# Kernel optimization log

Measured on AMD Instinct MI355X. Metric: run time of the kernel, lower is better.

Reference implementation:

```python
import jax, jax.numpy as jnp
import numpy as np

N_NODES = 50000
N_EDGES = 1600000
IN_DIM = 128
N_HEADS = 8
OUT_DIM = 16  # output_dim // n_heads = 128 // 8


def setup_inputs() -> dict:
    key = jax.random.key(0)
    ks = jax.random.split(key, 8)
    feature = jax.random.normal(ks[0], (N_NODES, IN_DIM), dtype=jnp.float32)
    edge_src = jax.random.randint(ks[1], (N_EDGES,), 0, N_NODES)
    edge_dst = jax.random.randint(ks[2], (N_EDGES,), 0, N_NODES)
    edge_weight = jax.random.uniform(ks[3], (N_EDGES,), dtype=jnp.float32)
    w_lin = jax.random.normal(ks[4], (IN_DIM, N_HEADS * OUT_DIM), dtype=jnp.float32) * 0.1
    att_l = jax.random.normal(ks[5], (N_HEADS, OUT_DIM), dtype=jnp.float32) * 0.1
    att_r = jax.random.normal(ks[6], (N_HEADS, OUT_DIM), dtype=jnp.float32) * 0.1
    w_res = jax.random.normal(ks[7], (IN_DIM, N_HEADS * OUT_DIM), dtype=jnp.float32) * 0.1
    return {"feature": feature, "edge_src": edge_src, "edge_dst": edge_dst,
            "edge_weight": edge_weight, "w_lin": w_lin, "att_l": att_l,
            "att_r": att_r, "w_res": w_res}


def reference(feature, edge_src, edge_dst, edge_weight, w_lin, att_l, att_r, w_res):
    N = feature.shape[0]
    H, C = att_l.shape
    # Linear projection -> [N, H, C]
    x = (feature @ w_lin).reshape(N, H, C)
    # Per-node attention logits [N, H]
    al = jnp.einsum('nhc,hc->nh', x, att_l)
    ar = jnp.einsum('nhc,hc->nh', x, att_r)
    # Per-edge logits: gather src/dst, weight, leaky-relu  [E, H]
    alpha = al[edge_src] + ar[edge_dst]
    alpha = edge_weight[:, None] * alpha
    alpha = jax.nn.leaky_relu(alpha, negative_slope=0.2)
    # Segment softmax over edges grouped by destination node
    m = jax.ops.segment_max(alpha, edge_dst, num_segments=N)  # [N, H]
    m = jnp.where(jnp.isfinite(m), m, 0.0)
    e = jnp.exp(alpha - m[edge_dst])
    denom = jax.ops.segment_sum(e, edge_dst, num_segments=N)  # [N, H]
    coef = e / denom[edge_dst]                                 # [E, H]
    # Message passing: gather src feats, weight by coef, scatter-sum to dst
    msg = x[edge_src] * coef[:, :, None]                       # [E, H, C]
    feat = jax.ops.segment_sum(msg, edge_dst, num_segments=N)  # [N, H, C]
    out = jax.nn.elu(feat).reshape(N, H * C)
    out = out + feature @ w_res  # residual branch
    return out
```

## Files before the change

kernel.cpp:

```cpp
#include <hip/hip_runtime.h>
#include <math.h>

#define IN_DIM 128
#define NH 8
#define OC 16
#define HC 128
#define BSTR 136
#define ECH 4096
#define BINSZ 128
#define NBINS_MAX 512
#define FSTR 132
#define ALS 32

typedef __attribute__((ext_vector_type(8))) short short8;
typedef __attribute__((ext_vector_type(4))) float f32x4;

__device__ __forceinline__ unsigned short bf16_rne(float f) {
  unsigned int u = __builtin_bit_cast(unsigned int, f);
  u += 0x7FFFu + ((u >> 16) & 1u);
  return (unsigned short)(u >> 16);
}
__device__ __forceinline__ float bf16_to_f(unsigned short h) {
  unsigned int u = ((unsigned int)h) << 16;
  return __builtin_bit_cast(float, u);
}

__global__ __launch_bounds__(256) void k1_fused(const float* __restrict__ feature,
                                                const float* __restrict__ w_lin,
                                                const float* __restrict__ w_res,
                                                const float* __restrict__ att_l,
                                                const float* __restrict__ att_r,
                                                unsigned char* __restrict__ x8,
                                                unsigned char* __restrict__ als,
                                                float* __restrict__ ar,
                                                float* __restrict__ out,
                                                int* __restrict__ bin_cursor, int N) {
  __shared__ unsigned short BL[HC * BSTR];
  __shared__ unsigned short BR[HC * BSTR];
  __shared__ unsigned short WH[16 * BSTR];
  __shared__ unsigned short WL[16 * BSTR];
  const int t = threadIdx.x;
  if (blockIdx.x == 0) {
    bin_cursor[t] = 0;
    bin_cursor[t + 256] = 0;
  }
  for (int i = t; i < IN_DIM * HC; i += 256) {
    const int r = i >> 7, c = i & 127;
    BL[c * BSTR + r] = bf16_rne(w_lin[i]);
    BR[c * BSTR + r] = bf16_rne(w_res[i]);
  }
#pragma unroll
  for (int j = 0; j < 8; ++j) {
    const int idx = t * 8 + j;
    const int k = idx >> 4, c = idx & 15;
    const int h8 = c & 7;
    const float* __restrict__ av = ((c < 8) ? att_l : att_r) + h8 * OC;
    const float* __restrict__ wr = w_lin + k * HC + h8 * OC;
    float acc = 0.f;
#pragma unroll
    for (int oc = 0; oc < 16; ++oc) acc = fmaf(wr[oc], av[oc], acc);
    const unsigned short hi = bf16_rne(acc);
    WH[c * BSTR + k] = hi;
    WL[c * BSTR + k] = bf16_rne(acc - bf16_to_f(hi));
  }
  __syncthreads();

  const int wave = t >> 6, lane = t & 63;
  const int n16 = lane & 15, quad = lane >> 4;
  const int nStrips = (N + 15) >> 4;

  for (int strip = blockIdx.x * 4 + wave; strip < nStrips; strip += gridDim.x * 4) {
    const int row0 = strip * 16;
    const int arow = row0 + n16;
    const float* __restrict__ ap =
        feature + (size_t)((arow < N) ? arow : 0) * IN_DIM + quad * 8;
    short8 ahi[4], alo[4];
#pragma unroll
    for (int ks = 0; ks < 4; ++ks) {
      const float4 f0 = *(const float4*)(ap + ks * 32);
      const float4 f1 = *(const float4*)(ap + ks * 32 + 4);
      const float fv[8] = {f0.x, f0.y, f0.z, f0.w, f1.x, f1.y, f1.z, f1.w};
      short8 h, l;
#pragma unroll
      for (int j = 0; j < 8; ++j) {
        const unsigned short hh = bf16_rne(fv[j]);
        h[j] = (short)hh;
        l[j] = (short)bf16_rne(fv[j] - bf16_to_f(hh));
      }
      ahi[ks] = h;
      alo[ks] = l;
    }
    f32x4 xacc[8];
#pragma unroll
    for (int u = 0; u < 8; ++u) xacc[u] = (f32x4){0.f, 0.f, 0.f, 0.f};
#pragma unroll
    for (int ks = 0; ks < 4; ++ks) {
#pragma unroll
      for (int u = 0; u < 8; ++u) {
        const int boff = (u * 16 + n16) * BSTR + ks * 32 + quad * 8;
        const short8 bh = *(const short8*)&BL[boff];
        xacc[u] = __builtin_amdgcn_mfma_f32_16x16x32_bf16(ahi[ks], bh, xacc[u], 0, 0, 0);
        xacc[u] = __builtin_amdgcn_mfma_f32_16x16x32_bf16(alo[ks], bh, xacc[u], 0, 0, 0);
      }
    }
    {
      f32x4 accA = {0.f, 0.f, 0.f, 0.f};
#pragma unroll
      for (int ks = 0; ks < 4; ++ks) {
        const int boff = n16 * BSTR + ks * 32 + quad * 8;
        const short8 wh = *(const short8*)&WH[boff];
        const short8 wl = *(const short8*)&WL[boff];
        accA = __builtin_amdgcn_mfma_f32_16x16x32_bf16(ahi[ks], wh, accA, 0, 0, 0);
        accA = __builtin_amdgcn_mfma_f32_16x16x32_bf16(alo[ks], wh, accA, 0, 0, 0);
        accA = __builtin_amdgcn_mfma_f32_16x16x32_bf16(ahi[ks], wl, accA, 0, 0, 0);
      }
#pragma unroll
      for (int r = 0; r < 4; ++r) {
        const int rr = row0 + quad * 4 + r;
        if (rr < N) {
          if (n16 < 8) {
            *(unsigned short*)(als + (size_t)rr * ALS + n16 * 2) = bf16_rne(accA[r]);
          } else {
            ar[(size_t)rr * NH + (n16 - 8)] = accA[r];
          }
        }
      }
    }
    float m[4];
#pragma unroll
    for (int r = 0; r < 4; ++r) {
      float mm = 0.f;
#pragma unroll
      for (int u = 0; u < 8; ++u) mm = fmaxf(mm, fabsf(xacc[u][r]));
      mm = fmaxf(mm, __shfl_xor(mm, 1));
      mm = fmaxf(mm, __shfl_xor(mm, 2));
      mm = fmaxf(mm, __shfl_xor(mm, 4));
      mm = fmaxf(mm, __shfl_xor(mm, 8));
      m[r] = mm;
    }
#pragma unroll
    for (int r = 0; r < 4; ++r) {
      const int rr = row0 + quad * 4 + r;
      if (rr < N) {
        const float inv = (m[r] > 0.f) ? 127.f / m[r] : 0.f;
#pragma unroll
        for (int u = 0; u < 8; ++u) {
          const int q8 = (int)rintf(xacc[u][r] * inv) + 128;
          x8[(size_t)rr * HC + u * 16 + n16] = (unsigned char)q8;
        }
        if (n16 == 0)
          *(float*)(als + (size_t)rr * ALS + 16) = (m[r] > 0.f) ? m[r] / 127.f : 0.f;
      }
    }
#pragma unroll
    for (int cg = 0; cg < 2; ++cg) {
      f32x4 acc[4] = {{0.f,0.f,0.f,0.f},{0.f,0.f,0.f,0.f},{0.f,0.f,0.f,0.f},{0.f,0.f,0.f,0.f}};
#pragma unroll
      for (int ks = 0; ks < 4; ++ks) {
#pragma unroll
        for (int j = 0; j < 4; ++j) {
          const int boff = ((cg * 4 + j) * 16 + n16) * BSTR + ks * 32 + quad * 8;
          const short8 bh = *(const short8*)&BR[boff];
          acc[j] = __builtin_amdgcn_mfma_f32_16x16x32_bf16(ahi[ks], bh, acc[j], 0, 0, 0);
          acc[j] = __builtin_amdgcn_mfma_f32_16x16x32_bf16(alo[ks], bh, acc[j], 0, 0, 0);
        }
      }
#pragma unroll
      for (int j = 0; j < 4; ++j) {
        const int colo = (cg * 4 + j) * 16 + n16;
#pragma unroll
        for (int r = 0; r < 4; ++r) {
          const int rr = row0 + quad * 4 + r;
          if (rr < N) out[(size_t)rr * HC + colo] = acc[j][r];
        }
      }
    }
  }
}

__global__ __launch_bounds__(1024) void kb1_scatter(const int* __restrict__ esrc,
                                                    const int* __restrict__ edst,
                                                    const float* __restrict__ ew,
                                                    int* __restrict__ bin_cursor,
                                                    uint2* __restrict__ tmp,
                                                    int E, int nbins, int cap) {
  __shared__ int cnt[NBINS_MAX];
  __shared__ int gbase[NBINS_MAX];
  const int t = threadIdx.x;
  if (t < NBINS_MAX) cnt[t] = 0;
  __syncthreads();
  const int base = blockIdx.x * ECH;
  uint2 v[4];
  int bj[4], sj[4];
#pragma unroll
  for (int j = 0; j < 4; ++j) {
    const int e = base + j * 1024 + t;
    bj[j] = -1;
    if (e < E) {
      const int d = edst[e];
      v[j] = make_uint2((unsigned)esrc[e] | ((unsigned)(d & (BINSZ - 1)) << 16),
                        __float_as_uint(ew[e]));
      bj[j] = d >> 7;
      sj[j] = atomicAdd(&cnt[bj[j]], 1);
    }
  }
  __syncthreads();
  for (int b = t; b < nbins; b += 1024) {
    const int own = cnt[b];
    if (own > 0) gbase[b] = atomicAdd(&bin_cursor[b], own);
  }
  __syncthreads();
#pragma unroll
  for (int j = 0; j < 4; ++j)
    if (bj[j] >= 0) {
      const int p = gbase[bj[j]] + sj[j];
      if (p >= 0 && p < cap) tmp[(size_t)bj[j] * cap + p] = v[j];
    }
}

__global__ __launch_bounds__(1024) void kb3_sort(const uint2* __restrict__ tmp,
                                                 const int* __restrict__ bin_cursor,
                                                 uint2* __restrict__ packed,
                                                 int* __restrict__ row_start,
                                                 int cap, int nbins, int N) {
  const int b = blockIdx.x, t = threadIdx.x;
  const int M = min(bin_cursor[b], cap);
  __shared__ int redw[16];
  int part = 0;
  for (int i = t; i < b; i += 1024) part += bin_cursor[i];
#pragma unroll
  for (int o = 32; o >= 1; o >>= 1) part += __shfl_xor(part, o);
  if ((t & 63) == 0) redw[t >> 6] = part;
  __syncthreads();
  int gstart = 0;
#pragma unroll
  for (int w = 0; w < 16; ++w) gstart += redw[w];
  if (b == nbins - 1 && t == 0) row_start[N] = gstart + M;

  const uint2* __restrict__ src = tmp + (size_t)b * cap;
  __shared__ int cnt[BINSZ];
  __shared__ int sbase[BINSZ];
  __shared__ int s[BINSZ];
  if (t < BINSZ) cnt[t] = 0;
  __syncthreads();
  uint2 v[6];
  int dj[6], sj[6];
#pragma unroll
  for (int j = 0; j < 6; ++j) {
    const int i = j * 1024 + t;
    dj[j] = -1;
    if (i < M) {
      v[j] = src[i];
      dj[j] = (int)(v[j].x >> 16);
      sj[j] = atomicAdd(&cnt[dj[j]], 1);
    }
  }
  __syncthreads();
  if (t < BINSZ) s[t] = cnt[t];
  __syncthreads();
  for (int o = 1; o < BINSZ; o <<= 1) {
    int a = 0;
    if (t < BINSZ && t >= o) a = s[t - o];
    __syncthreads();
    if (t < BINSZ) s[t] += a;
    __syncthreads();
  }
  if (t < BINSZ) {
    const int ex = s[t] - cnt[t];
    sbase[t] = gstart + ex;
    const int node = b * BINSZ + t;
    if (node < N) row_start[node] = gstart + ex;
  }
  __syncthreads();
#pragma unroll
  for (int j = 0; j < 6; ++j)
    if (dj[j] >= 0) packed[sbase[dj[j]] + sj[j]] = make_uint2(v[j].x & 0xFFFFu, v[j].y);
}

__global__ __launch_bounds__(64) void k5_agg(const unsigned char* __restrict__ x8,
                                             const unsigned char* __restrict__ als,
                                             const uint2* __restrict__ packed,
                                             const int* __restrict__ row_start,
                                             const float* __restrict__ ar,
                                             float* __restrict__ out, int N) {
  const int n = blockIdx.x;
  const int l = threadIdx.x;
  const int s0 = row_start[n];
  const int En = row_start[n + 1] - s0;
  if (En == 0) return;
  __shared__ int sbuf[64];
  __shared__ float wbuf[64];
  __shared__ float scbuf[64];
  __shared__ float fred[8 * FSTR];
  const int h = l & 7;
  const int g = l >> 3;
  const int ch0 = h * 16;

  const float arn = ar[(size_t)n * NH + h];
  float dpart = 0.f;
  float facsum = 0.f;
  float f[16];
#pragma unroll
  for (int j = 0; j < 16; ++j) f[j] = 0.f;

  for (int base = 0; base < En; base += 64) {
    const int cnt = min(64, En - base);
    __syncthreads();
    if (l < cnt) {
      const uint2 p = packed[s0 + base + l];
      const int src = (int)p.x;
      sbuf[l] = src;
      wbuf[l] = __uint_as_float(p.y);
      scbuf[l] = *(const float*)(als + (size_t)src * ALS + 16);
    }
    __syncthreads();
    for (int i = g; i < cnt; i += 8) {
      const int src = sbuf[i];
      const float aln =
          bf16_to_f(*(const unsigned short*)(als + (size_t)src * ALS + (h << 1)));
      float a = wbuf[i] * (aln + arn);
      a = (a > 0.f) ? a : 0.2f * a;
      const float e = __expf(a);
      dpart += e;
      const float fac = e * scbuf[i];
      facsum += fac;
      const int4 qw = *(const int4*)(x8 + (size_t)src * HC + ch0);
      const unsigned ux = (unsigned)qw.x, uy = (unsigned)qw.y;
      const unsigned uz = (unsigned)qw.z, uw = (unsigned)qw.w;
      f[0]  = fmaf(fac, (float)(ux & 0xFFu),         f[0]);
      f[1]  = fmaf(fac, (float)((ux >> 8) & 0xFFu),  f[1]);
      f[2]  = fmaf(fac, (float)((ux >> 16) & 0xFFu), f[2]);
      f[3]  = fmaf(fac, (float)(ux >> 24),           f[3]);
      f[4]  = fmaf(fac, (float)(uy & 0xFFu),         f[4]);
      f[5]  = fmaf(fac, (float)((uy >> 8) & 0xFFu),  f[5]);
      f[6]  = fmaf(fac, (float)((uy >> 16) & 0xFFu), f[6]);
      f[7]  = fmaf(fac, (float)(uy >> 24),           f[7]);
      f[8]  = fmaf(fac, (float)(uz & 0xFFu),         f[8]);
      f[9]  = fmaf(fac, (float)((uz >> 8) & 0xFFu),  f[9]);
      f[10] = fmaf(fac, (float)((uz >> 16) & 0xFFu), f[10]);
      f[11] = fmaf(fac, (float)(uz >> 24),           f[11]);
      f[12] = fmaf(fac, (float)(uw & 0xFFu),         f[12]);
      f[13] = fmaf(fac, (float)((uw >> 8) & 0xFFu),  f[13]);
      f[14] = fmaf(fac, (float)((uw >> 16) & 0xFFu), f[14]);
      f[15] = fmaf(fac, (float)(uw >> 24),           f[15]);
    }
  }
  dpart += __shfl_xor(dpart, 8);
  dpart += __shfl_xor(dpart, 16);
  dpart += __shfl_xor(dpart, 32);
  facsum += __shfl_xor(facsum, 8);
  facsum += __shfl_xor(facsum, 16);
  facsum += __shfl_xor(facsum, 32);
#pragma unroll
  for (int q = 0; q < 4; ++q) {
    const f32x4 v = {f[q * 4 + 0], f[q * 4 + 1], f[q * 4 + 2], f[q * 4 + 3]};
    *(f32x4*)&fred[g * FSTR + ch0 + q * 4] = v;
  }
  __syncthreads();
  float a0 = 0.f, a1 = 0.f;
#pragma unroll
  for (int gg = 0; gg < 8; ++gg) {
    const float2 v = *(const float2*)&fred[gg * FSTR + 2 * l];
    a0 += v.x;
    a1 += v.y;
  }
  const float dH = __shfl(dpart, l >> 3);
  const float fsH = __shfl(facsum, l >> 3);
  const float inv = 1.f / dH;
  float f0 = (a0 - 128.f * fsH) * inv;
  float f1 = (a1 - 128.f * fsH) * inv;
  f0 = (f0 > 0.f) ? f0 : (__expf(f0) - 1.f);
  f1 = (f1 > 0.f) ? f1 : (__expf(f1) - 1.f);
  float2 o = *(float2*)&out[(size_t)n * HC + 2 * l];
  o.x += f0;
  o.y += f1;
  *(float2*)&out[(size_t)n * HC + 2 * l] = o;
}

extern "C" void kernel_launch(void* const* d_in, const int* in_sizes, int n_in,
                              void* d_out, int out_size, void* d_ws, size_t ws_size,
                              hipStream_t stream) {
  const float* feature = (const float*)d_in[0];
  const int* esrc = (const int*)d_in[1];
  const int* edst = (const int*)d_in[2];
  const float* ew = (const float*)d_in[3];
  const float* w_lin = (const float*)d_in[4];
  const float* att_l = (const float*)d_in[5];
  const float* att_r = (const float*)d_in[6];
  const float* w_res = (const float*)d_in[7];
  float* out = (float*)d_out;

  const int N = in_sizes[0] / IN_DIM;
  const int E = in_sizes[1];
  const int nbins = (N + BINSZ - 1) / BINSZ;
  int cap = (E + nbins - 1) / nbins;
  cap = cap + cap / 4 + 512;
  cap = (cap + 63) & ~63;
  const int nch = (E + ECH - 1) / ECH;

  char* ws = (char*)d_ws;
  size_t off = 0;
  auto alloc = [&](size_t bytes) {
    void* p = ws + off;
    off = (off + bytes + 255) & ~(size_t)255;
    return p;
  };
  uint2* tmp = (uint2*)alloc((size_t)nbins * cap * sizeof(uint2));
  unsigned char* x8 = (unsigned char*)alloc((size_t)N * HC);
  unsigned char* als = (unsigned char*)alloc((size_t)N * ALS);
  float* ar = (float*)alloc((size_t)N * NH * sizeof(float));
  int* row_start = (int*)alloc((size_t)(N + 1) * sizeof(int));
  int* bin_cursor = (int*)alloc((size_t)NBINS_MAX * sizeof(int));
  uint2* packed = (uint2*)alloc((size_t)E * sizeof(uint2));

  k1_fused<<<512, 256, 0, stream>>>(feature, w_lin, w_res, att_l, att_r,
                                    x8, als, ar, out, bin_cursor, N);
  kb1_scatter<<<nch, 1024, 0, stream>>>(esrc, edst, ew, bin_cursor, tmp, E, nbins, cap);
  kb3_sort<<<nbins, 1024, 0, stream>>>(tmp, bin_cursor, packed, row_start, cap, nbins, N);
  k5_agg<<<N, 64, 0, stream>>>(x8, als, packed, row_start, ar, out, N);
}
```

Baseline: 192.5 us.

## Split projection kernel and co-schedule residual GEMM with edge binning

The fused projection kernel is split in two. One kernel computes x, the attention logits and the int8 quantisation using one strip per wave. A second kernel runs the residual GEMM and the edge-binning scatter together, with disjoint block ranges in a single launch, and the scatter now uses 256-thread blocks. The aim is to overlap the compute-bound residual matmul with the memory-bound binning and to drop the persistent grid-stride loop. In exchange the weights are converted into LDS once per block across many more blocks, and each scatter thread holds more registers.

After: 199.5 us. +3.6%, slower.

```diff
diff --git a/kernel.cpp b/kernel.cpp
--- a/kernel.cpp
+++ b/kernel.cpp
@@ -25,18 +25,15 @@
   return __builtin_bit_cast(float, u);
 }
 
-__global__ __launch_bounds__(256) void k1_fused(const float* __restrict__ feature,
-                                                const float* __restrict__ w_lin,
-                                                const float* __restrict__ w_res,
-                                                const float* __restrict__ att_l,
-                                                const float* __restrict__ att_r,
-                                                unsigned char* __restrict__ x8,
-                                                unsigned char* __restrict__ als,
-                                                float* __restrict__ ar,
-                                                float* __restrict__ out,
-                                                int* __restrict__ bin_cursor, int N) {
+__global__ __launch_bounds__(256) void k1a_x(const float* __restrict__ feature,
+                                             const float* __restrict__ w_lin,
+                                             const float* __restrict__ att_l,
+                                             const float* __restrict__ att_r,
+                                             unsigned char* __restrict__ x8,
+                                             unsigned char* __restrict__ als,
+                                             float* __restrict__ ar,
+                                             int* __restrict__ bin_cursor, int N) {
   __shared__ unsigned short BL[HC * BSTR];
-  __shared__ unsigned short BR[HC * BSTR];
   __shared__ unsigned short WH[16 * BSTR];
   __shared__ unsigned short WL[16 * BSTR];
   const int t = threadIdx.x;
@@ -47,7 +44,6 @@
   for (int i = t; i < IN_DIM * HC; i += 256) {
     const int r = i >> 7, c = i & 127;
     BL[c * BSTR + r] = bf16_rne(w_lin[i]);
-    BR[c * BSTR + r] = bf16_rne(w_res[i]);
   }
 #pragma unroll
   for (int j = 0; j < 8; ++j) {
@@ -68,8 +64,145 @@
   const int wave = t >> 6, lane = t & 63;
   const int n16 = lane & 15, quad = lane >> 4;
   const int nStrips = (N + 15) >> 4;
-
-  for (int strip = blockIdx.x * 4 + wave; strip < nStrips; strip += gridDim.x * 4) {
+  const int strip = blockIdx.x * 4 + wave;
+  if (strip >= nStrips) return;
+
+  const int row0 = strip * 16;
+  const int arow = row0 + n16;
+  const float* __restrict__ ap =
+      feature + (size_t)((arow < N) ? arow : 0) * IN_DIM + quad * 8;
+  short8 ahi[4], alo[4];
+#pragma unroll
+  for (int ks = 0; ks < 4; ++ks) {
+    const float4 f0 = *(const float4*)(ap + ks * 32);
+    const float4 f1 = *(const float4*)(ap + ks * 32 + 4);
+    const float fv[8] = {f0.x, f0.y, f0.z, f0.w, f1.x, f1.y, f1.z, f1.w};
+    short8 h, l;
+#pragma unroll
+    for (int j = 0; j < 8; ++j) {
+      const unsigned short hh = bf16_rne(fv[j]);
+      h[j] = (short)hh;
+      l[j] = (short)bf16_rne(fv[j] - bf16_to_f(hh));
+    }
+    ahi[ks] = h;
+    alo[ks] = l;
+  }
+  f32x4 xacc[8];
+#pragma unroll
+  for (int u = 0; u < 8; ++u) xacc[u] = (f32x4){0.f, 0.f, 0.f, 0.f};
+#pragma unroll
+  for (int ks = 0; ks < 4; ++ks) {
+#pragma unroll
+    for (int u = 0; u < 8; ++u) {
+      const int boff = (u * 16 + n16) * BSTR + ks * 32 + quad * 8;
+      const short8 bh = *(const short8*)&BL[boff];
+      xacc[u] = __builtin_amdgcn_mfma_f32_16x16x32_bf16(ahi[ks], bh, xacc[u], 0, 0, 0);
+      xacc[u] = __builtin_amdgcn_mfma_f32_16x16x32_bf16(alo[ks], bh, xacc[u], 0, 0, 0);
+    }
+  }
+  {
+    f32x4 accA = {0.f, 0.f, 0.f, 0.f};
+#pragma unroll
+    for (int ks = 0; ks < 4; ++ks) {
+      const int boff = n16 * BSTR + ks * 32 + quad * 8;
+      const short8 wh = *(const short8*)&WH[boff];
+      const short8 wl = *(const short8*)&WL[boff];
+      accA = __builtin_amdgcn_mfma_f32_16x16x32_bf16(ahi[ks], wh, accA, 0, 0, 0);
+      accA = __builtin_amdgcn_mfma_f32_16x16x32_bf16(alo[ks], wh, accA, 0, 0, 0);
+      accA = __builtin_amdgcn_mfma_f32_16x16x32_bf16(ahi[ks], wl, accA, 0, 0, 0);
+    }
+#pragma unroll
+    for (int r = 0; r < 4; ++r) {
+      const int rr = row0 + quad * 4 + r;
+      if (rr < N) {
+        if (n16 < 8) {
+          *(unsigned short*)(als + (size_t)rr * ALS + n16 * 2) = bf16_rne(accA[r]);
+        } else {
+          ar[(size_t)rr * NH + (n16 - 8)] = accA[r];
+        }
+      }
+    }
+  }
+#pragma unroll
+  for (int r = 0; r < 4; ++r) {
+    float mm = 0.f;
+#pragma unroll
+    for (int u = 0; u < 8; ++u) mm = fmaxf(mm, fabsf(xacc[u][r]));
+    mm = fmaxf(mm, __shfl_xor(mm, 1));
+    mm = fmaxf(mm, __shfl_xor(mm, 2));
+    mm = fmaxf(mm, __shfl_xor(mm, 4));
+    mm = fmaxf(mm, __shfl_xor(mm, 8));
+    const int rr = row0 + quad * 4 + r;
+    if (rr < N) {
+      const float inv = (mm > 0.f) ? 127.f / mm : 0.f;
+#pragma unroll
+      for (int u = 0; u < 8; ++u) {
+        const int q8 = (int)rintf(xacc[u][r] * inv) + 128;
+        x8[(size_t)rr * HC + u * 16 + n16] = (unsigned char)q8;
+      }
+      if (n16 == 0)
+        *(float*)(als + (size_t)rr * ALS + 16) = (mm > 0.f) ? mm / 127.f : 0.f;
+    }
+  }
+}
+
+__global__ __launch_bounds__(256) void k_res_bin(const float* __restrict__ feature,
+                                                 const float* __restrict__ w_res,
+                                                 const int* __restrict__ esrc,
+                                                 const int* __restrict__ edst,
+                                                 const float* __restrict__ ew,
+                                                 int* __restrict__ bin_cursor,
+                                                 uint2* __restrict__ tmp,
+                                                 float* __restrict__ out,
+                                                 int N, int E, int nbins, int cap,
+                                                 int nkb) {
+  __shared__ __align__(16) char smraw[HC * BSTR * 2];
+  const int t = threadIdx.x;
+  if (blockIdx.x < nkb) {
+    int* cnt = (int*)smraw;
+    int* gbase = cnt + NBINS_MAX;
+    cnt[t] = 0;
+    cnt[t + 256] = 0;
+    __syncthreads();
+    const int base = blockIdx.x * ECH;
+    uint2 v[16];
+    int bj[16], sj[16];
+#pragma unroll
+    for (int j = 0; j < 16; ++j) {
+      const int e = base + j * 256 + t;
+      bj[j] = -1;
+      if (e < E) {
+        const int d = edst[e];
+        v[j] = make_uint2((unsigned)esrc[e] | ((unsigned)(d & (BINSZ - 1)) << 16),
+                          __float_as_uint(ew[e]));
+        bj[j] = d >> 7;
+        sj[j] = atomicAdd(&cnt[bj[j]], 1);
+      }
+    }
+    __syncthreads();
+    for (int b = t; b < nbins; b += 256) {
+      const int own = cnt[b];
+      if (own > 0) gbase[b] = atomicAdd(&bin_cursor[b], own);
+    }
+    __syncthreads();
+#pragma unroll
+    for (int j = 0; j < 16; ++j)
+      if (bj[j] >= 0) {
+        const int p = gbase[bj[j]] + sj[j];
+        if (p >= 0 && p < cap) tmp[(size_t)bj[j] * cap + p] = v[j];
+      }
+  } else {
+    unsigned short* BR = (unsigned short*)smraw;
+    for (int i = t; i < IN_DIM * HC; i += 256) {
+      const int r = i >> 7, c = i & 127;
+      BR[c * BSTR + r] = bf16_rne(w_res[i]);
+    }
+    __syncthreads();
+    const int wave = t >> 6, lane = t & 63;
+    const int n16 = lane & 15, quad = lane >> 4;
+    const int nStrips = (N + 15) >> 4;
+    const int strip = (blockIdx.x - nkb) * 4 + wave;
+    if (strip >= nStrips) return;
     const int row0 = strip * 16;
     const int arow = row0 + n16;
     const float* __restrict__ ap =
@@ -89,68 +222,6 @@
       }
       ahi[ks] = h;
       alo[ks] = l;
-    }
-    f32x4 xacc[8];
-#pragma unroll
-    for (int u = 0; u < 8; ++u) xacc[u] = (f32x4){0.f, 0.f, 0.f, 0.f};
-#pragma unroll
-    for (int ks = 0; ks < 4; ++ks) {
-#pragma unroll
-      for (int u = 0; u < 8; ++u) {
-        const int boff = (u * 16 + n16) * BSTR + ks * 32 + quad * 8;
-        const short8 bh = *(const short8*)&BL[boff];
-        xacc[u] = __builtin_amdgcn_mfma_f32_16x16x32_bf16(ahi[ks], bh, xacc[u], 0, 0, 0);
-        xacc[u] = __builtin_amdgcn_mfma_f32_16x16x32_bf16(alo[ks], bh, xacc[u], 0, 0, 0);
-      }
-    }
-    {
-      f32x4 accA = {0.f, 0.f, 0.f, 0.f};
-#pragma unroll
-      for (int ks = 0; ks < 4; ++ks) {
-        const int boff = n16 * BSTR + ks * 32 + quad * 8;
-        const short8 wh = *(const short8*)&WH[boff];
-        const short8 wl = *(const short8*)&WL[boff];
-        accA = __builtin_amdgcn_mfma_f32_16x16x32_bf16(ahi[ks], wh, accA, 0, 0, 0);
-        accA = __builtin_amdgcn_mfma_f32_16x16x32_bf16(alo[ks], wh, accA, 0, 0, 0);
-        accA = __builtin_amdgcn_mfma_f32_16x16x32_bf16(ahi[ks], wl, accA, 0, 0, 0);
-      }
-#pragma unroll
-      for (int r = 0; r < 4; ++r) {
-        const int rr = row0 + quad * 4 + r;
-        if (rr < N) {
-          if (n16 < 8) {
-            *(unsigned short*)(als + (size_t)rr * ALS + n16 * 2) = bf16_rne(accA[r]);
-          } else {
-            ar[(size_t)rr * NH + (n16 - 8)] = accA[r];
-          }
-        }
-      }
-    }
-    float m[4];
-#pragma unroll
-    for (int r = 0; r < 4; ++r) {
-      float mm = 0.f;
-#pragma unroll
-      for (int u = 0; u < 8; ++u) mm = fmaxf(mm, fabsf(xacc[u][r]));
-      mm = fmaxf(mm, __shfl_xor(mm, 1));
-      mm = fmaxf(mm, __shfl_xor(mm, 2));
-      mm = fmaxf(mm, __shfl_xor(mm, 4));
-      mm = fmaxf(mm, __shfl_xor(mm, 8));
-      m[r] = mm;
-    }
-#pragma unroll
-    for (int r = 0; r < 4; ++r) {
-      const int rr = row0 + quad * 4 + r;
-      if (rr < N) {
-        const float inv = (m[r] > 0.f) ? 127.f / m[r] : 0.f;
-#pragma unroll
-        for (int u = 0; u < 8; ++u) {
-          const int q8 = (int)rintf(xacc[u][r] * inv) + 128;
-          x8[(size_t)rr * HC + u * 16 + n16] = (unsigned char)q8;
-        }
-        if (n16 == 0)
-          *(float*)(als + (size_t)rr * ALS + 16) = (m[r] > 0.f) ? m[r] / 127.f : 0.f;
-      }
     }
 #pragma unroll
     for (int cg = 0; cg < 2; ++cg) {
@@ -176,46 +247,6 @@
       }
     }
   }
-}
-
-__global__ __launch_bounds__(1024) void kb1_scatter(const int* __restrict__ esrc,
-                                                    const int* __restrict__ edst,
-                                                    const float* __restrict__ ew,
-                                                    int* __restrict__ bin_cursor,
-                                                    uint2* __restrict__ tmp,
-                                                    int E, int nbins, int cap) {
-  __shared__ int cnt[NBINS_MAX];
-  __shared__ int gbase[NBINS_MAX];
-  const int t = threadIdx.x;
-  if (t < NBINS_MAX) cnt[t] = 0;
-  __syncthreads();
-  const int base = blockIdx.x * ECH;
-  uint2 v[4];
-  int bj[4], sj[4];
-#pragma unroll
-  for (int j = 0; j < 4; ++j) {
-    const int e = base + j * 1024 + t;
-    bj[j] = -1;
-    if (e < E) {
-      const int d = edst[e];
-      v[j] = make_uint2((unsigned)esrc[e] | ((unsigned)(d & (BINSZ - 1)) << 16),
-                        __float_as_uint(ew[e]));
-      bj[j] = d >> 7;
-      sj[j] = atomicAdd(&cnt[bj[j]], 1);
-    }
-  }
-  __syncthreads();
-  for (int b = t; b < nbins; b += 1024) {
-    const int own = cnt[b];
-    if (own > 0) gbase[b] = atomicAdd(&bin_cursor[b], own);
-  }
-  __syncthreads();
-#pragma unroll
-  for (int j = 0; j < 4; ++j)
-    if (bj[j] >= 0) {
-      const int p = gbase[bj[j]] + sj[j];
-      if (p >= 0 && p < cap) tmp[(size_t)bj[j] * cap + p] = v[j];
-    }
 }
 
 __global__ __launch_bounds__(1024) void kb3_sort(const uint2* __restrict__ tmp,
@@ -396,7 +427,9 @@
   int cap = (E + nbins - 1) / nbins;
   cap = cap + cap / 4 + 512;
   cap = (cap + 63) & ~63;
-  const int nch = (E + ECH - 1) / ECH;
+  const int nkb = (E + ECH - 1) / ECH;
+  const int nStrips = (N + 15) >> 4;
+  const int nk1 = (nStrips + 3) / 4;
 
   char* ws = (char*)d_ws;
   size_t off = 0;
@@ -413,9 +446,11 @@
   int* bin_cursor = (int*)alloc((size_t)NBINS_MAX * sizeof(int));
   uint2* packed = (uint2*)alloc((size_t)E * sizeof(uint2));
 
-  k1_fused<<<512, 256, 0, stream>>>(feature, w_lin, w_res, att_l, att_r,
-                                    x8, als, ar, out, bin_cursor, N);
-  kb1_scatter<<<nch, 1024, 0, stream>>>(esrc, edst, ew, bin_cursor, tmp, E, nbins, cap);
+  k1a_x<<<nk1, 256, 0, stream>>>(feature, w_lin, att_l, att_r, x8, als, ar,
+                                 bin_cursor, N);
+  k_res_bin<<<nkb + nk1, 256, 0, stream>>>(feature, w_res, esrc, edst, ew,
+                                           bin_cursor, tmp, out, N, E, nbins,
+                                           cap, nkb);
   kb3_sort<<<nbins, 1024, 0, stream>>>(tmp, bin_cursor, packed, row_start, cap, nbins, N);
   k5_agg<<<N, 64, 0, stream>>>(x8, als, packed, row_start, ar, out, N);
 }
```
